# Kernel optimization log

Measured on AMD Instinct MI355X. Metric: run time of the kernel, lower is better.

Reference implementation:

```python
import jax, jax.numpy as jnp
import numpy as np

# ---- model hyperparameters (match init_kwargs) ----
D_MODEL = 1024
D_STATE = 128
EXPAND = 2
HEADDIM = 64
NGROUPS = 1
D_INNER = EXPAND * D_MODEL            # 2048
NHEADS = D_INNER // HEADDIM           # 32
ROPE_FRAC = 0.5
SPLIT = int(D_STATE * ROPE_FRAC)      # 64 rotary dims
NANG = SPLIT // 2                     # 32 rope angles
A_FLOOR = 1e-4
EPS = 1e-5
BATCH, SEQLEN = 1, 1024
SIZES = [D_INNER, D_INNER, D_STATE * NGROUPS, D_STATE * NGROUPS, NHEADS, NHEADS, NHEADS, NANG]
D_IN_PROJ = int(np.sum(SIZES))        # 4480


def setup_inputs() -> dict:
    key = jax.random.key(0)
    ks = jax.random.split(key, 6)
    u = jax.random.normal(ks[0], (BATCH, SEQLEN, D_MODEL), dtype=jnp.float32)
    W_in = jax.random.normal(ks[1], (D_MODEL, D_IN_PROJ), dtype=jnp.float32) * 0.02
    # dt_bias ~ log(dt) for dt in [1e-3, 0.1] -> around -4
    dt_bias = jax.random.normal(ks[2], (NHEADS,), dtype=jnp.float32) * 0.5 - 4.0
    B_bias = jnp.ones((NHEADS, D_STATE), jnp.float32) + 0.01 * jax.random.normal(ks[3], (NHEADS, D_STATE), dtype=jnp.float32)
    C_bias = jnp.ones((NHEADS, D_STATE), jnp.float32) + 0.01 * jax.random.normal(ks[4], (NHEADS, D_STATE), dtype=jnp.float32)
    Bn_w = jnp.ones((D_STATE,), jnp.float32)
    Cn_w = jnp.ones((D_STATE,), jnp.float32)
    D_param = jnp.ones((NHEADS,), jnp.float32)
    W_out = jax.random.normal(ks[5], (D_INNER, D_MODEL), dtype=jnp.float32) * 0.02
    return {"u": u, "W_in": W_in, "dt_bias": dt_bias, "B_bias": B_bias, "C_bias": C_bias,
            "Bn_w": Bn_w, "Cn_w": Cn_w, "D_param": D_param, "W_out": W_out}


def _rmsnorm(v, w):
    return v * jax.lax.rsqrt(jnp.mean(v * v, axis=-1, keepdims=True) + EPS) * w


def _forward(u, W_in, dt_bias, B_bias, C_bias, Bn_w, Cn_w, D_param, W_out):
    b, l, _ = u.shape
    proj = u @ W_in                                   # (b, l, d_in_proj)
    idx = np.cumsum(SIZES)[:-1]
    z, x, Bp, Cp, dd_dt, dd_A, trap_raw, ang = jnp.split(proj, idx, axis=-1)
    z = z.reshape(b, l, NHEADS, HEADDIM)
    x = x.reshape(b, l, NHEADS, HEADDIM)
    # A = clamp(-softplus(.), max=-A_floor);  dt = softplus(. + dt_bias)
    A = jnp.minimum(-jax.nn.softplus(dd_A), -A_FLOOR)          # (b,l,H)
    dt = jax.nn.softplus(dd_dt + dt_bias)                      # (b,l,H)
    a = jnp.exp(A * dt)                                        # decay per step
    lam = jax.nn.sigmoid(trap_raw)                             # trapezoid gate
    # RMSNorm on B/C (ngroups=1), then per-head additive bias
    Bn = _rmsnorm(Bp, Bn_w)                                    # (b,l,N)
    Cn = _rmsnorm(Cp, Cn_w)
    Bh = Bn[:, :, None, :] + B_bias                            # (b,l,H,N)
    Ch = Cn[:, :, None, :] + C_bias
    # data-dependent rotary: cumulative angle = cumsum(angles * dt)
    theta = jnp.cumsum(ang[:, :, None, :] * dt[..., None], axis=1)  # (b,l,H,NANG)
    cos, sin = jnp.cos(theta), jnp.sin(theta)

    def rope(v):
        d1, d2, rest = v[..., :NANG], v[..., NANG:SPLIT], v[..., SPLIT:]
        return jnp.concatenate([d1 * cos - d2 * sin, d1 * sin + d2 * cos, rest], axis=-1)

    Bh, Ch = rope(Bh), rope(Ch)

    tfirst = lambda v: jnp.moveaxis(v, 1, 0)
    inputs = (tfirst(Bh), tfirst(Ch), tfirst(x), tfirst(a), tfirst(dt), tfirst(lam))
    h0 = jnp.zeros((b, NHEADS, HEADDIM, D_STATE), jnp.float32)
    k0 = jnp.zeros((b, NHEADS, D_STATE), jnp.float32)
    v0 = jnp.zeros((b, NHEADS, HEADDIM), jnp.float32)

    def step(carry, inp):
        h, kp, vp = carry
        Bt, Ct, xt, at, dtt, lamt = inp
        # trapezoidal selective-scan update:
        # h_t = a_t h_{t-1} + dt_t (lam_t B_t x_t + (1-lam_t) a_t B_{t-1} x_{t-1})
        cur = jnp.einsum('bhp,bhn->bhpn', xt, Bt) * (dtt * lamt)[..., None, None]
        prv = jnp.einsum('bhp,bhn->bhpn', vp, kp) * (dtt * (1.0 - lamt) * at)[..., None, None]
        h = at[..., None, None] * h + cur + prv
        yt = jnp.einsum('bhn,bhpn->bhp', Ct, h)
        return (h, Bt, xt), yt

    _, y = jax.lax.scan(step, (h0, k0, v0), inputs)          # (l,b,H,P)
    y = jnp.moveaxis(y, 0, 1) + D_param[None, None, :, None] * x
    y = y * jax.nn.silu(z)                                    # gated output (no out-proj norm)
    return y.reshape(b, l, D_INNER) @ W_out


def reference(u, W_in, dt_bias, B_bias, C_bias, Bn_w, Cn_w, D_param, W_out):
    return _forward(u, W_in, dt_bias, B_bias, C_bias, Bn_w, Cn_w, D_param, W_out)
```

## Files before the change

kernel.cpp:

```cpp
#include <hip/hip_runtime.h>
#include <stdint.h>

#define SEQ     1024
#define DPROJ   4480

typedef __attribute__((ext_vector_type(8))) short short8;
typedef __attribute__((ext_vector_type(4))) float f4;

__device__ __forceinline__ short f2b(float f){
  union { float f; uint32_t u; } v; v.f = f;
  uint32_t r = (v.u + 0x7fffu + ((v.u >> 16) & 1u)) >> 16;
  return (short)(uint16_t)r;
}
__device__ __forceinline__ float b2f(uint16_t u){
  union { uint32_t u; float f; } v; v.u = ((uint32_t)u) << 16; return v.f;
}
__device__ __forceinline__ uint32_t pack2(float lo, float hi){
  return (uint32_t)(uint16_t)f2b(lo) | ((uint32_t)(uint16_t)f2b(hi) << 16);
}
__device__ __forceinline__ float softplus_f(float x){
  return x > 20.f ? x : log1pf(__expf(x));
}
__device__ __forceinline__ void gload_lds16(const short* g, short* l){
  __builtin_amdgcn_global_load_lds((const __attribute__((address_space(1))) void*)g,
                                   (__attribute__((address_space(3))) void*)l, 16, 0, 0);
}

__global__ __launch_bounds__(256) void prep_inputs(const float* __restrict__ u, short* __restrict__ u16,
                                                   const float* __restrict__ W_in, short* __restrict__ WtIn,
                                                   const float* __restrict__ W_out, short* __restrict__ WtOut,
                                                   float* __restrict__ outz){
  int b = blockIdx.x;
  int tid = threadIdx.x;
  if (b < 1024){
    int i = (b * 256 + tid) * 4;
    f4 v = *(const f4*)(u + i);
    uint2 pk; pk.x = pack2(v.x, v.y); pk.y = pack2(v.z, v.w);
    *(uint2*)(u16 + i) = pk;
    return;
  }
  if (b >= 2656){
    int i = ((b - 2656) * 256 + tid) * 4;
    *(f4*)(outz + i) = (f4){0.f, 0.f, 0.f, 0.f};
    return;
  }
  const float* in; short* outp; int R, lda, bx, by;
  if (b < 2144){ int idx = b - 1024; bx = idx % 140; by = idx / 140; in = W_in;  outp = WtIn;  R = 1024; lda = 4480; }
  else         { int idx = b - 2144; bx = idx & 31;  by = idx >> 5;  in = W_out; outp = WtOut; R = 2048; lda = 1024; }
  __shared__ float tile[32][132];
  int bc = bx * 32, br = by * 128;
  int c = tid & 31, r0 = tid >> 5;
  #pragma unroll
  for (int i = 0; i < 16; i++){
    int r = r0 + i * 8;
    tile[c][r] = in[(size_t)(br + r) * lda + bc + c];
  }
  __syncthreads();
  #pragma unroll
  for (int i = 0; i < 4; i++){
    int task = tid + 256 * i;
    int cc = task >> 5;
    int rg = (task & 31) * 4;
    f4 v = *(const f4*)&tile[cc][rg];
    uint2 pk; pk.x = pack2(v.x, v.y); pk.y = pack2(v.z, v.w);
    *(uint2*)(outp + (size_t)(bc + cc) * R + br + rg) = pk;
  }
}

__global__ __launch_bounds__(256) void gemm1_kernel(const short* __restrict__ A, const short* __restrict__ Bt,
                                                    float* __restrict__ C){
  const int N = 4480, K = 1024;
  __shared__ __align__(16) short As[2][128 * 32];
  __shared__ __align__(16) short Bs[2][160 * 32];
  const int tid  = threadIdx.x;
  const int wave = tid >> 6;
  const int lane = tid & 63;
  const int m0 = blockIdx.y * 128;
  const int n0 = blockIdx.x * 160;
  const int wm = (wave >> 1) * 64;
  const int wn = (wave & 1) * 80;
  const int quad = lane >> 4;
  const int r16  = lane & 15;

  f4 acc[4][5];
  #pragma unroll
  for (int i = 0; i < 4; i++)
    #pragma unroll
    for (int j = 0; j < 5; j++) acc[i][j] = (f4){0.f, 0.f, 0.f, 0.f};

  const int row0 = tid >> 2;
  const int kq   = tid & 3;
  const short* gA0 = A  + (size_t)(m0 + row0) * K + kq * 8;
  const short* gA1 = A  + (size_t)(m0 + row0 + 64) * K + kq * 8;
  const short* gB0 = Bt + (size_t)(n0 + row0) * K + kq * 8;
  const short* gB1 = Bt + (size_t)(n0 + row0 + 64) * K + kq * 8;
  const short* gB2 = Bt + (size_t)(n0 + row0 + 128) * K + kq * 8;

  gload_lds16(gA0, &As[0][(size_t)tid * 8]);
  gload_lds16(gA1, &As[0][(size_t)(tid + 256) * 8]);
  gload_lds16(gB0, &Bs[0][(size_t)tid * 8]);
  gload_lds16(gB1, &Bs[0][(size_t)(tid + 256) * 8]);
  if (tid < 128) gload_lds16(gB2, &Bs[0][(size_t)(tid + 512) * 8]);

  for (int kt = 0; kt < 32; ++kt){
    const int cur = kt & 1;
    __syncthreads();
    if (kt + 1 < 32){
      const int ko = (kt + 1) * 32;
      const int nxt = cur ^ 1;
      gload_lds16(gA0 + ko, &As[nxt][(size_t)tid * 8]);
      gload_lds16(gA1 + ko, &As[nxt][(size_t)(tid + 256) * 8]);
      gload_lds16(gB0 + ko, &Bs[nxt][(size_t)tid * 8]);
      gload_lds16(gB1 + ko, &Bs[nxt][(size_t)(tid + 256) * 8]);
      if (tid < 128) gload_lds16(gB2 + ko, &Bs[nxt][(size_t)(tid + 512) * 8]);
    }
    short8 af[4], bf[5];
    #pragma unroll
    for (int i = 0; i < 4; i++)
      af[i] = *(const short8*)&As[cur][(wm + i * 16 + r16) * 32 + quad * 8];
    #pragma unroll
    for (int j = 0; j < 5; j++)
      bf[j] = *(const short8*)&Bs[cur][(wn + j * 16 + r16) * 32 + quad * 8];
    #pragma unroll
    for (int i = 0; i < 4; i++)
      #pragma unroll
      for (int j = 0; j < 5; j++)
        acc[i][j] = __builtin_amdgcn_mfma_f32_16x16x32_bf16(af[i], bf[j], acc[i][j], 0, 0, 0);
  }

  #pragma unroll
  for (int i = 0; i < 4; i++)
    #pragma unroll
    for (int j = 0; j < 5; j++)
      #pragma unroll
      for (int rr = 0; rr < 4; ++rr){
        int row = m0 + wm + i * 16 + quad * 4 + rr;
        int col = n0 + wn + j * 16 + r16;
        C[(size_t)row * N + col] = acc[i][j][rr];
      }
}

__global__ __launch_bounds__(256) void gemm2_kernel(const short* __restrict__ A, const short* __restrict__ Bt,
                                                    float* __restrict__ C){
  const int N = 1024, K = 2048, klen = 512;
  __shared__ __align__(16) short As[2][128 * 32];
  __shared__ __align__(16) short Bs[2][128 * 32];
  const int tid  = threadIdx.x;
  const int wave = tid >> 6;
  const int lane = tid & 63;
  const int m0 = blockIdx.y * 128;
  const int n0 = blockIdx.x * 128;
  const int k0 = blockIdx.z * klen;
  const int wm = (wave >> 1) * 64;
  const int wn = (wave & 1) * 64;
  const int quad = lane >> 4;
  const int r16  = lane & 15;

  f4 acc[4][4];
  #pragma unroll
  for (int i = 0; i < 4; i++)
    #pragma unroll
    for (int j = 0; j < 4; j++) acc[i][j] = (f4){0.f, 0.f, 0.f, 0.f};

  const int row0 = tid >> 2;
  const int kq   = tid & 3;
  const short* gA0 = A  + (size_t)(m0 + row0) * K + k0 + kq * 8;
  const short* gA1 = A  + (size_t)(m0 + row0 + 64) * K + k0 + kq * 8;
  const short* gB0 = Bt + (size_t)(n0 + row0) * K + k0 + kq * 8;
  const short* gB1 = Bt + (size_t)(n0 + row0 + 64) * K + k0 + kq * 8;

  gload_lds16(gA0, &As[0][(size_t)tid * 8]);
  gload_lds16(gA1, &As[0][(size_t)(tid + 256) * 8]);
  gload_lds16(gB0, &Bs[0][(size_t)tid * 8]);
  gload_lds16(gB1, &Bs[0][(size_t)(tid + 256) * 8]);

  for (int kt = 0; kt < klen / 32; ++kt){
    const int cur = kt & 1;
    __syncthreads();
    if (kt + 1 < klen / 32){
      const int ko = (kt + 1) * 32;
      const int nxt = cur ^ 1;
      gload_lds16(gA0 + ko, &As[nxt][(size_t)tid * 8]);
      gload_lds16(gA1 + ko, &As[nxt][(size_t)(tid + 256) * 8]);
      gload_lds16(gB0 + ko, &Bs[nxt][(size_t)tid * 8]);
      gload_lds16(gB1 + ko, &Bs[nxt][(size_t)(tid + 256) * 8]);
    }
    short8 af[4], bf[4];
    #pragma unroll
    for (int i = 0; i < 4; i++){
      af[i] = *(const short8*)&As[cur][(wm + i * 16 + r16) * 32 + quad * 8];
      bf[i] = *(const short8*)&Bs[cur][(wn + i * 16 + r16) * 32 + quad * 8];
    }
    #pragma unroll
    for (int i = 0; i < 4; i++)
      #pragma unroll
      for (int j = 0; j < 4; j++)
        acc[i][j] = __builtin_amdgcn_mfma_f32_16x16x32_bf16(af[i], bf[j], acc[i][j], 0, 0, 0);
  }

  #pragma unroll
  for (int i = 0; i < 4; i++)
    #pragma unroll
    for (int j = 0; j < 4; j++)
      #pragma unroll
      for (int rr = 0; rr < 4; ++rr){
        int row = m0 + wm + i * 16 + quad * 4 + rr;
        int col = n0 + wn + j * 16 + r16;
        unsafeAtomicAdd(&C[(size_t)row * N + col], acc[i][j][rr]);
      }
}

__global__ __launch_bounds__(256) void scan_theta(const float* __restrict__ proj,
                                                  const float* __restrict__ dt_bias,
                                                  float* __restrict__ Lcum, float* __restrict__ u2b,
                                                  float* __restrict__ c1b,
                                                  float* __restrict__ cosb, float* __restrict__ sinb){
  int b = blockIdx.x;
  int tid = threadIdx.x;
  int t0 = tid * 4;
  int lane = tid & 63, wave = tid >> 6;
  __shared__ float wsum[4];
  if (b < 32){
    int h = b;
    float dtbias = dt_bias[h];
    float dt5[5], lam5[5];
    #pragma unroll
    for (int i = 0; i < 5; i++){
      int t = t0 + i;
      if (t < 1024){
        const float* row = proj + (size_t)t * DPROJ;
        dt5[i]  = softplus_f(row[4352 + h] + dtbias);
        lam5[i] = 1.f / (1.f + __expf(-row[4416 + h]));
      } else { dt5[i] = 0.f; lam5[i] = 0.f; }
    }
    float v[4], c1[4], c2n[4];
    #pragma unroll
    for (int i = 0; i < 4; i++){
      int t = t0 + i;
      const float* row = proj + (size_t)t * DPROJ;
      float Ah = -fmaxf(softplus_f(row[4384 + h]), 1e-4f);
      v[i]   = Ah * dt5[i];
      c1[i]  = dt5[i] * lam5[i];
      c2n[i] = dt5[i + 1] * (1.f - lam5[i + 1]);
    }
    v[1] += v[0]; v[2] += v[1]; v[3] += v[2];
    float tot = v[3], sc = tot;
    #pragma unroll
    for (int off = 1; off < 64; off <<= 1){
      float n = __shfl_up(sc, off, 64);
      if (lane >= off) sc += n;
    }
    if (lane == 63) wsum[wave] = sc;
    __syncthreads();
    float base = sc - tot;
    for (int w = 0; w < wave; ++w) base += wsum[w];
    #pragma unroll
    for (int i = 0; i < 4; i++){
      int t = t0 + i;
      Lcum[h * 1024 + t] = base + v[i];
      u2b[h * 1024 + t]  = c1[i] + c2n[i];
      c1b[h * 1024 + t]  = c1[i];
    }
  } else {
    int hk = b - 32;
    int h = hk >> 5, k = hk & 31;
    float dtbias = dt_bias[h];
    float v[4];
    #pragma unroll
    for (int i = 0; i < 4; i++){
      const float* row = proj + (size_t)(t0 + i) * DPROJ;
      float dt = softplus_f(row[4352 + h] + dtbias);
      v[i] = row[4448 + k] * dt;
    }
    v[1] += v[0]; v[2] += v[1]; v[3] += v[2];
    float tot = v[3], sc = tot;
    #pragma unroll
    for (int off = 1; off < 64; off <<= 1){
      float n = __shfl_up(sc, off, 64);
      if (lane >= off) sc += n;
    }
    if (lane == 63) wsum[wave] = sc;
    __syncthreads();
    float base = sc - tot;
    for (int w = 0; w < wave; ++w) base += wsum[w];
    #pragma unroll
    for (int i = 0; i < 4; i++){
      float th = base + v[i];
      float s, c;
      __sincosf(th, &s, &c);
      int t = t0 + i;
      cosb[(size_t)t * 1024 + h * 32 + k] = c;
      sinb[(size_t)t * 1024 + h * 32 + k] = s;
    }
  }
}

__global__ __launch_bounds__(256) void bcxt_kernel(const float* __restrict__ proj,
                                                   const float* __restrict__ B_bias, const float* __restrict__ C_bias,
                                                   const float* __restrict__ Bn_w, const float* __restrict__ Cn_w,
                                                   const float* __restrict__ cosb, const float* __restrict__ sinb,
                                                   short* __restrict__ Bb, short* __restrict__ Cb,
                                                   short* __restrict__ xTb){
  int b = blockIdx.x;
  int tid = threadIdx.x;
  if (b >= 1024){
    int idx = b - 1024;
    int bx = idx & 63, by = idx >> 6;
    __shared__ float tile[32][132];
    int bc = bx * 32, br = by * 128;
    int c = tid & 31, r0 = tid >> 5;
    #pragma unroll
    for (int i = 0; i < 16; i++){
      int r = r0 + i * 8;
      tile[c][r] = proj[(size_t)(br + r) * 4480 + 2048 + bc + c];
    }
    __syncthreads();
    #pragma unroll
    for (int i = 0; i < 4; i++){
      int task = tid + 256 * i;
      int cc = task >> 5;
      int rg = (task & 31) * 4;
      f4 v = *(const f4*)&tile[cc][rg];
      uint2 pk; pk.x = pack2(v.x, v.y); pk.y = pack2(v.z, v.w);
      *(uint2*)(xTb + (size_t)(bc + cc) * 1024 + br + rg) = pk;
    }
    return;
  }
  int t = b;
  __shared__ float vv[2][128];
  __shared__ float red[4];
  int n = tid & 127;
  int isC = tid >> 7;
  float val = proj[(size_t)t * DPROJ + 4096 + isC * 128 + n];
  float ss = val * val;
  #pragma unroll
  for (int off = 32; off >= 1; off >>= 1) ss += __shfl_down(ss, off);
  int wave = tid >> 6, lane = tid & 63;
  if (lane == 0) red[wave] = ss;
  __syncthreads();
  float rsv = isC ? rsqrtf((red[2] + red[3]) * (1.f / 128.f) + 1e-5f)
                  : rsqrtf((red[0] + red[1]) * (1.f / 128.f) + 1e-5f);
  vv[isC][n] = val * rsv * (isC ? Cn_w[n] : Bn_w[n]);
  __syncthreads();
  const float* cb = cosb + (size_t)t * 1024;
  const float* sb = sinb + (size_t)t * 1024;
  #pragma unroll
  for (int it = 0; it < 8; it++){
    int task = tid + 256 * it;
    int arr  = task >> 10;
    int rem  = task & 1023;
    int h    = rem >> 5;
    int n0   = (rem & 31) * 4;
    const float* bias = arr ? C_bias : B_bias;
    const float* base = vv[arr];
    f4 bv = *(const f4*)&base[n0];
    f4 bi = *(const f4*)&bias[h * 128 + n0];
    f4 o;
    if (n0 < 32){
      f4 bv2 = *(const f4*)&base[n0 + 32];
      f4 bi2 = *(const f4*)&bias[h * 128 + n0 + 32];
      f4 cv = *(const f4*)&cb[h * 32 + n0];
      f4 sv = *(const f4*)&sb[h * 32 + n0];
      #pragma unroll
      for (int q = 0; q < 4; q++) o[q] = (bv[q] + bi[q]) * cv[q] - (bv2[q] + bi2[q]) * sv[q];
    } else if (n0 < 64){
      int k0 = n0 - 32;
      f4 bv1 = *(const f4*)&base[k0];
      f4 bi1 = *(const f4*)&bias[h * 128 + k0];
      f4 cv = *(const f4*)&cb[h * 32 + k0];
      f4 sv = *(const f4*)&sb[h * 32 + k0];
      #pragma unroll
      for (int q = 0; q < 4; q++) o[q] = (bv1[q] + bi1[q]) * sv[q] + (bv[q] + bi[q]) * cv[q];
    } else {
      #pragma unroll
      for (int q = 0; q < 4; q++) o[q] = bv[q] + bi[q];
    }
    uint2 pk; pk.x = pack2(o.x, o.y); pk.y = pack2(o.z, o.w);
    short* outp = arr ? Cb : Bb;
    *(uint2*)(outp + (size_t)t * 4096 + h * 128 + n0) = pk;
  }
}

__global__ __launch_bounds__(256) void hpart_kernel(const short* __restrict__ xTb, const short* __restrict__ Bb,
                                                    const float* __restrict__ Lcum, const float* __restrict__ u2b,
                                                    short* __restrict__ Hpart){
  int h = blockIdx.x >> 3, c = blockIdx.x & 7;
  int t0 = c * 128;
  int tid = threadIdx.x;
  __shared__ float wS[128];
  if (tid < 128){
    float Lend = Lcum[h * 1024 + t0 + 127];
    wS[tid] = __expf(Lend - Lcum[h * 1024 + t0 + tid]) * u2b[h * 1024 + t0 + tid];
  }
  __syncthreads();
  int wave = tid >> 6, lane = tid & 63, quad = lane >> 4, r16 = lane & 15;
  int n0 = wave * 32;
  f4 acc[4][2];
  #pragma unroll
  for (int i = 0; i < 4; i++)
    #pragma unroll
    for (int j = 0; j < 2; j++) acc[i][j] = (f4){0.f, 0.f, 0.f, 0.f};

  const ushort* Bh = (const ushort*)Bb + (size_t)t0 * 4096 + h * 128;
  #pragma unroll
  for (int kk = 0; kk < 4; ++kk){
    int sb = kk * 32 + quad * 8;
    short8 af[4];
    #pragma unroll
    for (int i = 0; i < 4; i++){
      int p = i * 16 + r16;
      af[i] = *(const short8*)(xTb + (size_t)(h * 64 + p) * 1024 + t0 + sb);
    }
    float wv[8];
    #pragma unroll
    for (int jj = 0; jj < 8; jj++) wv[jj] = wS[sb + jj];
    short8 bfr[2];
    #pragma unroll
    for (int j = 0; j < 2; j++){
      int nn = n0 + j * 16 + r16;
      float e[8];
      #pragma unroll
      for (int jj = 0; jj < 8; jj++)
        e[jj] = b2f(Bh[(size_t)(sb + jj) * 4096 + nn]) * wv[jj];
      union { short8 s; uint32_t u[4]; } fr;
      #pragma unroll
      for (int q = 0; q < 4; q++) fr.u[q] = pack2(e[2 * q], e[2 * q + 1]);
      bfr[j] = fr.s;
    }
    #pragma unroll
    for (int i = 0; i < 4; i++)
      #pragma unroll
      for (int j = 0; j < 2; j++)
        acc[i][j] = __builtin_amdgcn_mfma_f32_16x16x32_bf16(af[i], bfr[j], acc[i][j], 0, 0, 0);
  }

  short* out = Hpart + ((size_t)(h * 8 + c)) * 8192;
  #pragma unroll
  for (int i = 0; i < 4; i++)
    #pragma unroll
    for (int rr = 0; rr < 4; ++rr){
      int p = i * 16 + quad * 4 + rr;
      #pragma unroll
      for (int j = 0; j < 2; j++){
        int nn = n0 + j * 16 + r16;
        out[p * 128 + nn] = f2b(acc[i][j][rr]);
      }
    }
}

__global__ __launch_bounds__(256) void hscan_kernel(const short* __restrict__ Hpart,
                                                    const float* __restrict__ Lcum,
                                                    short* __restrict__ Hused){
  int idx = blockIdx.x * 256 + threadIdx.x;
  int h = idx >> 13, rem = idx & 8191;
  float acc = 0.f;
  float Lprev = 0.f;
  #pragma unroll
  for (int c = 0; c < 8; c++){
    Hused[((size_t)(h * 8 + c)) * 8192 + rem] = f2b(acc);
    float Lend = Lcum[h * 1024 + c * 128 + 127];
    float dec = __expf(Lend - Lprev);
    acc = dec * acc + b2f((uint16_t)Hpart[((size_t)(h * 8 + c)) * 8192 + rem]);
    Lprev = Lend;
  }
}

#define GS 144
__global__ __launch_bounds__(256) void chunky_kernel(const short* __restrict__ Cb, const short* __restrict__ Bbg,
                                                     const short* __restrict__ xTb, const short* __restrict__ Hused,
                                                     const float* __restrict__ Lcum, const float* __restrict__ u2b,
                                                     const float* __restrict__ c1b,
                                                     const float* __restrict__ proj, const float* __restrict__ D_par,
                                                     short* __restrict__ yb16){
  int h = blockIdx.x >> 3, c = blockIdx.x & 7;
  int t0 = c * 128;
  __shared__ __align__(16) short Gt[128 * GS];
  __shared__ float Lc[128], u2v[128], c1v[128];
  int tid = threadIdx.x;
  if (tid < 128){
    Lc[tid]  = Lcum[h * 1024 + t0 + tid];
    u2v[tid] = u2b[h * 1024 + t0 + tid];
    c1v[tid] = c1b[h * 1024 + t0 + tid];
  }
  float Lprev = (c > 0) ? Lcum[h * 1024 + t0 - 1] : 0.f;
  float Dp = D_par[h];
  int wave = tid >> 6, lane = tid & 63, quad = lane >> 4, r16 = lane & 15;
  int wm = (wave >> 1) * 64, wn = (wave & 1) * 64;

  f4 acc[4][4];
  #pragma unroll
  for (int i = 0; i < 4; i++)
    #pragma unroll
    for (int j = 0; j < 4; j++) acc[i][j] = (f4){0.f, 0.f, 0.f, 0.f};
  #pragma unroll
  for (int kk = 0; kk < 4; ++kk){
    short8 af[4], bf[4];
    #pragma unroll
    for (int i = 0; i < 4; i++)
      af[i] = *(const short8*)(Cb + (size_t)(t0 + wm + i * 16 + r16) * 4096 + h * 128 + kk * 32 + quad * 8);
    #pragma unroll
    for (int j = 0; j < 4; j++)
      bf[j] = *(const short8*)(Bbg + (size_t)(t0 + wn + j * 16 + r16) * 4096 + h * 128 + kk * 32 + quad * 8);
    #pragma unroll
    for (int i = 0; i < 4; i++)
      #pragma unroll
      for (int j = 0; j < 4; j++)
        acc[i][j] = __builtin_amdgcn_mfma_f32_16x16x32_bf16(af[i], bf[j], acc[i][j], 0, 0, 0);
  }
  __syncthreads();

  #pragma unroll
  for (int i = 0; i < 4; i++){
    #pragma unroll
    for (int rr = 0; rr < 4; ++rr){
      int trow = wm + i * 16 + quad * 4 + rr;
      float Lt = Lc[trow];
      #pragma unroll
      for (int j = 0; j < 4; j++){
        int scol = wn + j * 16 + r16;
        float g = 0.f;
        if (scol <= trow){
          float wcoef = (scol == trow) ? c1v[scol] : u2v[scol];
          g = acc[i][j][rr] * wcoef * __expf(Lt - Lc[scol]);
        }
        Gt[trow * GS + scol] = f2b(g);
      }
    }
  }
  __syncthreads();

  f4 accY[2][4], accZ[2][4];
  #pragma unroll
  for (int i = 0; i < 2; i++)
    #pragma unroll
    for (int j = 0; j < 4; j++){ accY[i][j] = (f4){0.f,0.f,0.f,0.f}; accZ[i][j] = (f4){0.f,0.f,0.f,0.f}; }
  int m0 = wave * 32;
  #pragma unroll
  for (int kk = 0; kk < 4; ++kk){
    short8 ag[2], ac[2], bx[4], bh[4];
    #pragma unroll
    for (int i = 0; i < 2; i++){
      ag[i] = *(const short8*)&Gt[(m0 + i * 16 + r16) * GS + kk * 32 + quad * 8];
      ac[i] = *(const short8*)(Cb + (size_t)(t0 + m0 + i * 16 + r16) * 4096 + h * 128 + kk * 32 + quad * 8);
    }
    #pragma unroll
    for (int j = 0; j < 4; j++){
      bx[j] = *(const short8*)(xTb + (size_t)(h * 64 + j * 16 + r16) * 1024 + t0 + kk * 32 + quad * 8);
      bh[j] = *(const short8*)(Hused + ((size_t)(h * 8 + c) * 64 + j * 16 + r16) * 128 + kk * 32 + quad * 8);
    }
    #pragma unroll
    for (int i = 0; i < 2; i++)
      #pragma unroll
      for (int j = 0; j < 4; j++){
        accY[i][j] = __builtin_amdgcn_mfma_f32_16x16x32_bf16(ag[i], bx[j], accY[i][j], 0, 0, 0);
        accZ[i][j] = __builtin_amdgcn_mfma_f32_16x16x32_bf16(ac[i], bh[j], accZ[i][j], 0, 0, 0);
      }
  }
  #pragma unroll
  for (int i = 0; i < 2; i++)
    #pragma unroll
    for (int rr = 0; rr < 4; ++rr){
      int trow = m0 + i * 16 + quad * 4 + rr;
      float ei = __expf(Lc[trow] - Lprev);
      const float* prow = proj + (size_t)(t0 + trow) * DPROJ;
      #pragma unroll
      for (int j = 0; j < 4; j++){
        int col = h * 64 + j * 16 + r16;
        float zv = prow[col];
        float xv = prow[2048 + col];
        float yv = accY[i][j][rr] + ei * accZ[i][j][rr] + Dp * xv;
        float o = yv * (zv / (1.f + __expf(-zv)));
        yb16[(size_t)(t0 + trow) * 2048 + col] = f2b(o);
      }
    }
}

extern "C" void kernel_launch(void* const* d_in, const int* in_sizes, int n_in,
                              void* d_out, int out_size, void* d_ws, size_t ws_size,
                              hipStream_t stream){
  const float* u       = (const float*)d_in[0];
  const float* W_in    = (const float*)d_in[1];
  const float* dt_bias = (const float*)d_in[2];
  const float* B_bias  = (const float*)d_in[3];
  const float* C_bias  = (const float*)d_in[4];
  const float* Bn_w    = (const float*)d_in[5];
  const float* Cn_w    = (const float*)d_in[6];
  const float* D_par   = (const float*)d_in[7];
  const float* W_out   = (const float*)d_in[8];
  float* out = (float*)d_out;

  char* ws = (char*)d_ws;
  short* u16   = (short*)(ws + 0);
  short* WtIn  = (short*)(ws + 2097152);
  short* WtOut = (short*)(ws + 11272192);
  float* proj  = (float*)(ws + 15466496);
  float* cosb  = (float*)(ws + 33816576);
  float* sinb  = (float*)(ws + 38010880);
  short* Bb    = (short*)(ws + 42205184);
  short* Cb    = (short*)(ws + 50593792);
  short* xTb   = (short*)(ws + 58982400);
  float* Lcum  = (float*)(ws + 63176704);
  float* u2b   = (float*)(ws + 63307776);
  float* c1b   = (float*)(ws + 63438848);
  short* Hpart = (short*)(ws + 63569920);
  short* Hused = (short*)(ws + 67764224);
  short* yb16  = (short*)(ws + 71958528);

  prep_inputs<<<3680, 256, 0, stream>>>(u, u16, W_in, WtIn, W_out, WtOut, out);
  gemm1_kernel<<<dim3(28, 8), 256, 0, stream>>>(u16, WtIn, proj);
  scan_theta<<<1056, 256, 0, stream>>>(proj, dt_bias, Lcum, u2b, c1b, cosb, sinb);
  bcxt_kernel<<<1536, 256, 0, stream>>>(proj, B_bias, C_bias, Bn_w, Cn_w, cosb, sinb, Bb, Cb, xTb);
  hpart_kernel<<<256, 256, 0, stream>>>(xTb, Bb, Lcum, u2b, Hpart);
  hscan_kernel<<<1024, 256, 0, stream>>>(Hpart, Lcum, Hused);
  chunky_kernel<<<256, 256, 0, stream>>>(Cb, Bb, xTb, Hused, Lcum, u2b, c1b, proj, D_par, yb16);
  gemm2_kernel<<<dim3(8, 8, 4), 256, 0, stream>>>(yb16, WtOut, out);
}
```

Baseline: 200.8 us.

## Fuse x transpose into GEMM epilogue, store z/x as bf16, inline inter-chunk state scan

The input-projection GEMM now writes z and x as bf16 plus a transposed bf16 copy of x, and puts the small tail columns (B, C, dt, A, trap, angles) into a compact fp32 buffer. This removes the separate transpose blocks from the B/C kernel and cuts fp32 proj traffic. The hscan kernel is dropped: each chunky block now rebuilds its starting state from the earlier chunk partials, with decay, directly into swizzled LDS. That removes one launch and the Hused round trip, at the cost of redundant per-block accumulation, a larger LDS footprint, and bf16 rounding of z and x.

```diff
diff --git a/kernel.cpp b/kernel.cpp
--- a/kernel.cpp
+++ b/kernel.cpp
@@ -2,7 +2,6 @@
 #include <stdint.h>
 
 #define SEQ     1024
-#define DPROJ   4480
 
 typedef __attribute__((ext_vector_type(8))) short short8;
 typedef __attribute__((ext_vector_type(4))) float f4;
@@ -68,8 +67,9 @@
 }
 
 __global__ __launch_bounds__(256) void gemm1_kernel(const short* __restrict__ A, const short* __restrict__ Bt,
-                                                    float* __restrict__ C){
-  const int N = 4480, K = 1024;
+                                                    short* __restrict__ zx, short* __restrict__ xTb,
+                                                    float* __restrict__ projT){
+  const int K = 1024;
   __shared__ __align__(16) short As[2][128 * 32];
   __shared__ __align__(16) short Bs[2][160 * 32];
   const int tid  = threadIdx.x;
@@ -131,13 +131,25 @@
   #pragma unroll
   for (int i = 0; i < 4; i++)
     #pragma unroll
-    for (int j = 0; j < 5; j++)
-      #pragma unroll
-      for (int rr = 0; rr < 4; ++rr){
-        int row = m0 + wm + i * 16 + quad * 4 + rr;
-        int col = n0 + wn + j * 16 + r16;
-        C[(size_t)row * N + col] = acc[i][j][rr];
+    for (int j = 0; j < 5; j++){
+      int colb = n0 + wn + j * 16 + r16;
+      int rowb = m0 + wm + i * 16 + quad * 4;
+      if (colb < 2048){
+        #pragma unroll
+        for (int rr = 0; rr < 4; ++rr)
+          zx[(size_t)(rowb + rr) * 4096 + colb] = f2b(acc[i][j][rr]);
+      } else if (colb < 4096){
+        uint2 pk; pk.x = pack2(acc[i][j][0], acc[i][j][1]); pk.y = pack2(acc[i][j][2], acc[i][j][3]);
+        *(uint2*)(xTb + (size_t)(colb - 2048) * 1024 + rowb) = pk;
+        #pragma unroll
+        for (int rr = 0; rr < 4; ++rr)
+          zx[(size_t)(rowb + rr) * 4096 + colb] = f2b(acc[i][j][rr]);
+      } else {
+        #pragma unroll
+        for (int rr = 0; rr < 4; ++rr)
+          projT[(size_t)(rowb + rr) * 384 + (colb - 4096)] = acc[i][j][rr];
       }
+    }
 }
 
 __global__ __launch_bounds__(256) void gemm2_kernel(const short* __restrict__ A, const short* __restrict__ Bt,
@@ -210,7 +222,7 @@
       }
 }
 
-__global__ __launch_bounds__(256) void scan_theta(const float* __restrict__ proj,
+__global__ __launch_bounds__(256) void scan_theta(const float* __restrict__ projT,
                                                   const float* __restrict__ dt_bias,
                                                   float* __restrict__ Lcum, float* __restrict__ u2b,
                                                   float* __restrict__ c1b,
@@ -228,17 +240,17 @@
     for (int i = 0; i < 5; i++){
       int t = t0 + i;
       if (t < 1024){
-        const float* row = proj + (size_t)t * DPROJ;
-        dt5[i]  = softplus_f(row[4352 + h] + dtbias);
-        lam5[i] = 1.f / (1.f + __expf(-row[4416 + h]));
+        const float* row = projT + (size_t)t * 384;
+        dt5[i]  = softplus_f(row[256 + h] + dtbias);
+        lam5[i] = 1.f / (1.f + __expf(-row[320 + h]));
       } else { dt5[i] = 0.f; lam5[i] = 0.f; }
     }
     float v[4], c1[4], c2n[4];
     #pragma unroll
     for (int i = 0; i < 4; i++){
       int t = t0 + i;
-      const float* row = proj + (size_t)t * DPROJ;
-      float Ah = -fmaxf(softplus_f(row[4384 + h]), 1e-4f);
+      const float* row = projT + (size_t)t * 384;
+      float Ah = -fmaxf(softplus_f(row[288 + h]), 1e-4f);
       v[i]   = Ah * dt5[i];
       c1[i]  = dt5[i] * lam5[i];
       c2n[i] = dt5[i + 1] * (1.f - lam5[i + 1]);
@@ -268,9 +280,9 @@
     float v[4];
     #pragma unroll
     for (int i = 0; i < 4; i++){
-      const float* row = proj + (size_t)(t0 + i) * DPROJ;
-      float dt = softplus_f(row[4352 + h] + dtbias);
-      v[i] = row[4448 + k] * dt;
+      const float* row = projT + (size_t)(t0 + i) * 384;
+      float dt = softplus_f(row[256 + h] + dtbias);
+      v[i] = row[352 + k] * dt;
     }
     v[1] += v[0]; v[2] += v[1]; v[3] += v[2];
     float tot = v[3], sc = tot;
@@ -295,43 +307,18 @@
   }
 }
 
-__global__ __launch_bounds__(256) void bcxt_kernel(const float* __restrict__ proj,
+__global__ __launch_bounds__(256) void bcxt_kernel(const float* __restrict__ projT,
                                                    const float* __restrict__ B_bias, const float* __restrict__ C_bias,
                                                    const float* __restrict__ Bn_w, const float* __restrict__ Cn_w,
                                                    const float* __restrict__ cosb, const float* __restrict__ sinb,
-                                                   short* __restrict__ Bb, short* __restrict__ Cb,
-                                                   short* __restrict__ xTb){
-  int b = blockIdx.x;
+                                                   short* __restrict__ Bb, short* __restrict__ Cb){
+  int t = blockIdx.x;
   int tid = threadIdx.x;
-  if (b >= 1024){
-    int idx = b - 1024;
-    int bx = idx & 63, by = idx >> 6;
-    __shared__ float tile[32][132];
-    int bc = bx * 32, br = by * 128;
-    int c = tid & 31, r0 = tid >> 5;
-    #pragma unroll
-    for (int i = 0; i < 16; i++){
-      int r = r0 + i * 8;
-      tile[c][r] = proj[(size_t)(br + r) * 4480 + 2048 + bc + c];
-    }
-    __syncthreads();
-    #pragma unroll
-    for (int i = 0; i < 4; i++){
-      int task = tid + 256 * i;
-      int cc = task >> 5;
-      int rg = (task & 31) * 4;
-      f4 v = *(const f4*)&tile[cc][rg];
-      uint2 pk; pk.x = pack2(v.x, v.y); pk.y = pack2(v.z, v.w);
-      *(uint2*)(xTb + (size_t)(bc + cc) * 1024 + br + rg) = pk;
-    }
-    return;
-  }
-  int t = b;
   __shared__ float vv[2][128];
   __shared__ float red[4];
   int n = tid & 127;
   int isC = tid >> 7;
-  float val = proj[(size_t)t * DPROJ + 4096 + isC * 128 + n];
+  float val = projT[(size_t)t * 384 + isC * 128 + n];
   float ss = val * val;
   #pragma unroll
   for (int off = 32; off >= 1; off >>= 1) ss += __shfl_down(ss, off);
@@ -448,33 +435,17 @@
     }
 }
 
-__global__ __launch_bounds__(256) void hscan_kernel(const short* __restrict__ Hpart,
-                                                    const float* __restrict__ Lcum,
-                                                    short* __restrict__ Hused){
-  int idx = blockIdx.x * 256 + threadIdx.x;
-  int h = idx >> 13, rem = idx & 8191;
-  float acc = 0.f;
-  float Lprev = 0.f;
-  #pragma unroll
-  for (int c = 0; c < 8; c++){
-    Hused[((size_t)(h * 8 + c)) * 8192 + rem] = f2b(acc);
-    float Lend = Lcum[h * 1024 + c * 128 + 127];
-    float dec = __expf(Lend - Lprev);
-    acc = dec * acc + b2f((uint16_t)Hpart[((size_t)(h * 8 + c)) * 8192 + rem]);
-    Lprev = Lend;
-  }
-}
-
 #define GS 144
 __global__ __launch_bounds__(256) void chunky_kernel(const short* __restrict__ Cb, const short* __restrict__ Bbg,
-                                                     const short* __restrict__ xTb, const short* __restrict__ Hused,
+                                                     const short* __restrict__ xTb, const short* __restrict__ Hpart,
                                                      const float* __restrict__ Lcum, const float* __restrict__ u2b,
                                                      const float* __restrict__ c1b,
-                                                     const float* __restrict__ proj, const float* __restrict__ D_par,
+                                                     const short* __restrict__ zx, const float* __restrict__ D_par,
                                                      short* __restrict__ yb16){
   int h = blockIdx.x >> 3, c = blockIdx.x & 7;
   int t0 = c * 128;
   __shared__ __align__(16) short Gt[128 * GS];
+  __shared__ __align__(16) short Hu[64 * 128];
   __shared__ float Lc[128], u2v[128], c1v[128];
   int tid = threadIdx.x;
   if (tid < 128){
@@ -484,6 +455,33 @@
   }
   float Lprev = (c > 0) ? Lcum[h * 1024 + t0 - 1] : 0.f;
   float Dp = D_par[h];
+
+  {
+    float hacc[32];
+    #pragma unroll
+    for (int q = 0; q < 32; q++) hacc[q] = 0.f;
+    for (int cp = 0; cp < c; ++cp){
+      float dec = __expf(Lprev - Lcum[h * 1024 + cp * 128 + 127]);
+      const short8* hp = (const short8*)((const ushort*)Hpart + ((size_t)(h * 8 + cp)) * 8192 + tid * 32);
+      #pragma unroll
+      for (int q = 0; q < 4; q++){
+        short8 v = hp[q];
+        #pragma unroll
+        for (int e = 0; e < 8; e++) hacc[q * 8 + e] += dec * b2f((uint16_t)v[e]);
+      }
+    }
+    int p = tid >> 2;
+    int wbase = tid * 64;
+    #pragma unroll
+    for (int q = 0; q < 4; q++){
+      union { short8 s; uint32_t u[4]; } fr;
+      #pragma unroll
+      for (int p2 = 0; p2 < 4; p2++) fr.u[p2] = pack2(hacc[q * 8 + p2 * 2], hacc[q * 8 + p2 * 2 + 1]);
+      int off = (wbase + q * 16) ^ ((p & 7) << 4);
+      *(short8*)((char*)Hu + off) = fr.s;
+    }
+  }
+
   int wave = tid >> 6, lane = tid & 63, quad = lane >> 4, r16 = lane & 15;
   int wm = (wave >> 1) * 64, wn = (wave & 1) * 64;
 
@@ -546,7 +544,9 @@
     #pragma unroll
     for (int j = 0; j < 4; j++){
       bx[j] = *(const short8*)(xTb + (size_t)(h * 64 + j * 16 + r16) * 1024 + t0 + kk * 32 + quad * 8);
-      bh[j] = *(const short8*)(Hused + ((size_t)(h * 8 + c) * 64 + j * 16 + r16) * 128 + kk * 32 + quad * 8);
+      int hrow = j * 16 + r16;
+      int hoff = (hrow * 256 + kk * 64 + quad * 16) ^ ((hrow & 7) << 4);
+      bh[j] = *(const short8*)((const char*)Hu + hoff);
     }
     #pragma unroll
     for (int i = 0; i < 2; i++)
@@ -556,18 +556,19 @@
         accZ[i][j] = __builtin_amdgcn_mfma_f32_16x16x32_bf16(ac[i], bh[j], accZ[i][j], 0, 0, 0);
       }
   }
+  const ushort* zxu = (const ushort*)zx;
   #pragma unroll
   for (int i = 0; i < 2; i++)
     #pragma unroll
     for (int rr = 0; rr < 4; ++rr){
       int trow = m0 + i * 16 + quad * 4 + rr;
       float ei = __expf(Lc[trow] - Lprev);
-      const float* prow = proj + (size_t)(t0 + trow) * DPROJ;
+      const ushort* zrow = zxu + (size_t)(t0 + trow) * 4096;
       #pragma unroll
       for (int j = 0; j < 4; j++){
         int col = h * 64 + j * 16 + r16;
-        float zv = prow[col];
-        float xv = prow[2048 + col];
+        float zv = b2f(zrow[col]);
+        float xv = b2f(zrow[2048 + col]);
         float yv = accY[i][j][rr] + ei * accZ[i][j][rr] + Dp * xv;
         float o = yv * (zv / (1.f + __expf(-zv)));
         yb16[(size_t)(t0 + trow) * 2048 + col] = f2b(o);
@@ -593,25 +594,24 @@
   short* u16   = (short*)(ws + 0);
   short* WtIn  = (short*)(ws + 2097152);
   short* WtOut = (short*)(ws + 11272192);
-  float* proj  = (float*)(ws + 15466496);
-  float* cosb  = (float*)(ws + 33816576);
-  float* sinb  = (float*)(ws + 38010880);
-  short* Bb    = (short*)(ws + 42205184);
-  short* Cb    = (short*)(ws + 50593792);
-  short* xTb   = (short*)(ws + 58982400);
-  float* Lcum  = (float*)(ws + 63176704);
-  float* u2b   = (float*)(ws + 63307776);
-  float* c1b   = (float*)(ws + 63438848);
-  short* Hpart = (short*)(ws + 63569920);
-  short* Hused = (short*)(ws + 67764224);
-  short* yb16  = (short*)(ws + 71958528);
+  short* zx    = (short*)(ws + 15466496);
+  float* projT = (float*)(ws + 23855104);
+  float* cosb  = (float*)(ws + 25427968);
+  float* sinb  = (float*)(ws + 29622272);
+  short* Bb    = (short*)(ws + 33816576);
+  short* Cb    = (short*)(ws + 42205184);
+  short* xTb   = (short*)(ws + 50593792);
+  float* Lcum  = (float*)(ws + 54788096);
+  float* u2b   = (float*)(ws + 54919168);
+  float* c1b   = (float*)(ws + 55050240);
+  short* Hpart = (short*)(ws + 55181312);
+  short* yb16  = (short*)(ws + 59375616);
 
   prep_inputs<<<3680, 256, 0, stream>>>(u, u16, W_in, WtIn, W_out, WtOut, out);
-  gemm1_kernel<<<dim3(28, 8), 256, 0, stream>>>(u16, WtIn, proj);
-  scan_theta<<<1056, 256, 0, stream>>>(proj, dt_bias, Lcum, u2b, c1b, cosb, sinb);
-  bcxt_kernel<<<1536, 256, 0, stream>>>(proj, B_bias, C_bias, Bn_w, Cn_w, cosb, sinb, Bb, Cb, xTb);
+  gemm1_kernel<<<dim3(28, 8), 256, 0, stream>>>(u16, WtIn, zx, xTb, projT);
+  scan_theta<<<1056, 256, 0, stream>>>(projT, dt_bias, Lcum, u2b, c1b, cosb, sinb);
+  bcxt_kernel<<<1024, 256, 0, stream>>>(projT, B_bias, C_bias, Bn_w, Cn_w, cosb, sinb, Bb, Cb);
   hpart_kernel<<<256, 256, 0, stream>>>(xTb, Bb, Lcum, u2b, Hpart);
-  hscan_kernel<<<1024, 256, 0, stream>>>(Hpart, Lcum, Hused);
-  chunky_kernel<<<256, 256, 0, stream>>>(Cb, Bb, xTb, Hused, Lcum, u2b, c1b, proj, D_par, yb16);
+  chunky_kernel<<<256, 256, 0, stream>>>(Cb, Bb, xTb, Hpart, Lcum, u2b, c1b, zx, D_par, yb16);
   gemm2_kernel<<<dim3(8, 8, 4), 256, 0, stream>>>(yb16, WtOut, out);
 }
```

New measurement: 201.7 us. About the same (+0.5%).
